# Optimization experiments

Measured on AMD Instinct MI355X. Metric: run time of the kernel, lower is better.

The kernel has to match this reference:

```python
import jax, jax.numpy as jnp
import numpy as np

N_NODES = 100000
N_EDGES = 2000000
H = 128


def setup_inputs() -> dict:
    key = jax.random.key(0)
    ks = jax.random.split(key, 5)
    z_src = jax.random.normal(ks[0], (N_NODES, H), dtype=jnp.float32)
    z_dst = jax.random.normal(ks[1], (N_NODES, H), dtype=jnp.float32)
    edge_label_index = jax.random.randint(ks[2], (2, N_EDGES), 0, N_NODES, dtype=jnp.int64)
    # Linear(2H, H) and Linear(H, 1) params (stored as [in, out] for x @ W)
    W1 = jax.random.normal(ks[3], (2 * H, H), dtype=jnp.float32) * (1.0 / np.sqrt(2 * H))
    b1 = jnp.zeros((H,), dtype=jnp.float32)
    W2 = jax.random.normal(ks[4], (H, 1), dtype=jnp.float32) * (1.0 / np.sqrt(H))
    b2 = jnp.zeros((1,), dtype=jnp.float32)
    return {"z_src": z_src, "z_dst": z_dst, "edge_label_index": edge_label_index,
            "W1": W1, "b1": b1, "W2": W2, "b2": b2}


def reference(z_src, z_dst, edge_label_index, W1, b1, W2, b2):
    row, col = edge_label_index[0], edge_label_index[1]
    # gather + concat -> [E, 2H]
    z = jnp.concatenate([z_src[row], z_dst[col]], axis=-1)
    h = jax.nn.relu(z @ W1 + b1)          # [E, H]
    out = h @ W2 + b2                     # [E, 1]
    return out.reshape(-1)
```

## Files before the change

### kernel.cpp

```cpp
#include <hip/hip_runtime.h>

#define HDIM 128
#define ZP   136
#define NBH  512

typedef __bf16 bf16_t;
typedef bf16_t bf16x8 __attribute__((ext_vector_type(8)));
typedef float  f32x4  __attribute__((ext_vector_type(4)));

__device__ __forceinline__ unsigned short f2bf_rne(float f) {
    unsigned int u = __float_as_uint(f);
    u += 0x7fffu + ((u >> 16) & 1u);
    return (unsigned short)(u >> 16);
}
__device__ __forceinline__ unsigned int pk_bf2(float a, float b) {
    return (unsigned int)f2bf_rne(a) | ((unsigned int)f2bf_rne(b) << 16);
}

__global__ __launch_bounds__(256) void convert_w1(
    const float* __restrict__ W1, unsigned short* __restrict__ Wt)
{
    const int o = blockIdx.x * 256 + threadIdx.x;
    const int g = o >> 14, rem = o & 16383, n = rem >> 7, k = rem & 127;
    Wt[o] = f2bf_rne(W1[g * 16384 + k * 128 + n]);
}

__global__ __launch_bounds__(256) void node_gemm_v3(
    const float* __restrict__ Zs, const float* __restrict__ Zd,
    const unsigned short* __restrict__ Wt, const float* __restrict__ b1,
    unsigned short* __restrict__ Abuf, unsigned short* __restrict__ Bbuf,
    int M)
{
    __shared__ unsigned short wlds[128 * ZP];

    const bool second = (blockIdx.x >= NBH);
    const float* __restrict__ Z          = second ? Zd : Zs;
    const unsigned short* __restrict__ W = Wt + (second ? 128 * 128 : 0);
    unsigned short* __restrict__ C       = second ? Bbuf : Abuf;
    const int bx = second ? (blockIdx.x - NBH) : blockIdx.x;
    const int t  = threadIdx.x;

    #pragma unroll
    for (int j = 0; j < 8; ++j) {
        const int u = t + 256 * j;
        const int n = u >> 4, c = u & 15;
        const uint4 v = *reinterpret_cast<const uint4*>(W + n * 128 + c * 8);
        *reinterpret_cast<uint4*>(wlds + n * ZP + c * 8) = v;
    }
    __syncthreads();

    const int lane = t & 63;
    const int wave = t >> 6;
    const int m    = lane & 15;
    const int quad = lane >> 4;

    const int ntiles = (M + 63) >> 6;
    for (int tile = bx; tile < ntiles; tile += NBH) {
        const int row0 = tile * 64;
        const int r    = row0 + wave * 16 + m;
        const int rc   = (r < M) ? r : (M - 1);
        const float* zrow = Z + (size_t)rc * HDIM;

        f32x4 acc[8] = {};
        #pragma unroll
        for (int ks = 0; ks < 4; ++ks) {
            const float4 v0 = *reinterpret_cast<const float4*>(zrow + ks * 32 + quad * 8);
            const float4 v1 = *reinterpret_cast<const float4*>(zrow + ks * 32 + quad * 8 + 4);
            union { unsigned int u[4]; bf16x8 h; } zf;
            zf.u[0] = pk_bf2(v0.x, v0.y);
            zf.u[1] = pk_bf2(v0.z, v0.w);
            zf.u[2] = pk_bf2(v1.x, v1.y);
            zf.u[3] = pk_bf2(v1.z, v1.w);
            #pragma unroll
            for (int ct = 0; ct < 8; ++ct) {
                const bf16x8 wf = *reinterpret_cast<const bf16x8*>(
                    wlds + (ct * 16 + m) * ZP + ks * 32 + quad * 8);
                acc[ct] = __builtin_amdgcn_mfma_f32_16x16x32_bf16(wf, zf.h, acc[ct], 0, 0, 0);
            }
        }

        if (r < M) {
            unsigned short* crow = C + (size_t)r * HDIM;
            #pragma unroll
            for (int ct = 0; ct < 8; ++ct) {
                const int col = ct * 16 + quad * 4;
                float4 bv = make_float4(0.f, 0.f, 0.f, 0.f);
                if (second) bv = *reinterpret_cast<const float4*>(b1 + col);
                uint2 o;
                o.x = pk_bf2(acc[ct][0] + bv.x, acc[ct][1] + bv.y);
                o.y = pk_bf2(acc[ct][2] + bv.z, acc[ct][3] + bv.w);
                *reinterpret_cast<uint2*>(crow + col) = o;
            }
        }
    }
}

__global__ __launch_bounds__(256) void edge_decode_bf16(
    const unsigned short* __restrict__ A, const unsigned short* __restrict__ Bm,
    const int* __restrict__ idx,
    const float* __restrict__ W2, const float* __restrict__ b2,
    float* __restrict__ out, int E)
{
    const int t   = threadIdx.x;
    const int sub = t & 15;
    const int grp = t >> 4;

    float w2r[8];
    #pragma unroll
    for (int i = 0; i < 8; ++i) w2r[i] = W2[sub * 8 + i];
    const float b2s = b2[0];

    const int stride = gridDim.x * 16;
    for (int e = blockIdx.x * 16 + grp; e < E; e += stride) {
        const int r = idx[e];
        const int c = idx[E + e];
        const uint4 av = *reinterpret_cast<const uint4*>(A  + (size_t)r * HDIM + sub * 8);
        const uint4 bv = *reinterpret_cast<const uint4*>(Bm + (size_t)c * HDIM + sub * 8);

        float s = 0.f;
        #pragma unroll
        for (int i = 0; i < 4; ++i) {
            const unsigned int ua = (&av.x)[i];
            const unsigned int ub = (&bv.x)[i];
            s += fmaxf(__uint_as_float(ua << 16)         + __uint_as_float(ub << 16),         0.f) * w2r[2 * i];
            s += fmaxf(__uint_as_float(ua & 0xffff0000u) + __uint_as_float(ub & 0xffff0000u), 0.f) * w2r[2 * i + 1];
        }
        s += __shfl_xor(s, 1);
        s += __shfl_xor(s, 2);
        s += __shfl_xor(s, 4);
        s += __shfl_xor(s, 8);
        if (sub == 0) out[e] = s + b2s;
    }
}

extern "C" void kernel_launch(void* const* d_in, const int* in_sizes, int n_in,
                              void* d_out, int out_size, void* d_ws, size_t ws_size,
                              hipStream_t stream)
{
    const float* z_src = (const float*)d_in[0];
    const float* z_dst = (const float*)d_in[1];
    const int*   eidx  = (const int*)d_in[2];
    const float* W1    = (const float*)d_in[3];
    const float* b1    = (const float*)d_in[4];
    const float* W2    = (const float*)d_in[5];
    const float* b2    = (const float*)d_in[6];
    float*       outp  = (float*)d_out;

    const int Nn = in_sizes[0] / HDIM;
    const int E  = in_sizes[2] / 2;

    unsigned short* Abuf = (unsigned short*)d_ws;
    unsigned short* Bbuf = Abuf + (size_t)Nn * HDIM;
    unsigned short* Wt   = Bbuf + (size_t)Nn * HDIM;

    convert_w1<<<128, 256, 0, stream>>>(W1, Wt);

    node_gemm_v3<<<2 * NBH, 256, 0, stream>>>(z_src, z_dst, Wt, b1, Abuf, Bbuf, Nn);

    edge_decode_bf16<<<8192, 256, 0, stream>>>(Abuf, Bbuf, eidx, W2, b2, outp, E);
}
```

Baseline: 292.2 us.

## Bucket-sort edges by source node before decode to improve gather locality

Adds a counting-sort pipeline (histogram, scan, atomic scatter) that groups edges into buckets of 128 source nodes, storing (row, col, edge id) records. The decode kernel then reads these sorted records so that source-row gathers from A hit cache better, and writes its output scattered by the original edge id. This adds four kernel launches, extra passes over the index array, a 32 MB sorted buffer, global atomics, and scattered output writes. The destination-side gathers stay random.

Result: slower. 766.7 us (+162.4%).

```diff
diff --git a/kernel.cpp b/kernel.cpp
--- a/kernel.cpp
+++ b/kernel.cpp
@@ -1,8 +1,9 @@
 #include <hip/hip_runtime.h>
 
-#define HDIM 128
-#define ZP   136
-#define NBH  512
+#define HDIM  128
+#define ZP    136
+#define NBH   512
+#define NBUCK 1024
 
 typedef __bf16 bf16_t;
 typedef bf16_t bf16x8 __attribute__((ext_vector_type(8)));
@@ -56,9 +57,8 @@
 
     const int ntiles = (M + 63) >> 6;
     for (int tile = bx; tile < ntiles; tile += NBH) {
-        const int row0 = tile * 64;
-        const int r    = row0 + wave * 16 + m;
-        const int rc   = (r < M) ? r : (M - 1);
+        const int r  = tile * 64 + wave * 16 + m;
+        const int rc = (r < M) ? r : (M - 1);
         const float* zrow = Z + (size_t)rc * HDIM;
 
         f32x4 acc[8] = {};
@@ -95,9 +95,58 @@
     }
 }
 
-__global__ __launch_bounds__(256) void edge_decode_bf16(
+__global__ __launch_bounds__(256) void zero_buf(int* __restrict__ p, int n)
+{
+    const int i = blockIdx.x * 256 + threadIdx.x;
+    if (i < n) p[i] = 0;
+}
+
+__global__ __launch_bounds__(256) void edge_hist(
+    const int* __restrict__ idx, int E, int* __restrict__ hist)
+{
+    __shared__ int h[NBUCK];
+    for (int i = threadIdx.x; i < NBUCK; i += 256) h[i] = 0;
+    __syncthreads();
+    const int stride = gridDim.x * 256;
+    for (int e = blockIdx.x * 256 + threadIdx.x; e < E; e += stride)
+        atomicAdd(&h[idx[e] >> 7], 1);
+    __syncthreads();
+    for (int i = threadIdx.x; i < NBUCK; i += 256)
+        if (h[i]) atomicAdd(&hist[i], h[i]);
+}
+
+__global__ __launch_bounds__(1024) void scan_hist(
+    const int* __restrict__ hist, int* __restrict__ cursor)
+{
+    __shared__ int a[NBUCK], b[NBUCK];
+    const int t = threadIdx.x;
+    a[t] = hist[t];
+    __syncthreads();
+    int* src = a; int* dst = b;
+    for (int off = 1; off < NBUCK; off <<= 1) {
+        dst[t] = (t >= off) ? (src[t - off] + src[t]) : src[t];
+        __syncthreads();
+        int* tmp = src; src = dst; dst = tmp;
+    }
+    cursor[t] = (t == 0) ? 0 : src[t - 1];
+}
+
+__global__ __launch_bounds__(256) void edge_scatter(
+    const int* __restrict__ idx, int E, int* __restrict__ cursor,
+    uint4* __restrict__ sorted)
+{
+    const int stride = gridDim.x * 256;
+    for (int e = blockIdx.x * 256 + threadIdx.x; e < E; e += stride) {
+        const int r = idx[e];
+        const int c = idx[E + e];
+        const int pos = atomicAdd(&cursor[r >> 7], 1);
+        sorted[pos] = make_uint4((unsigned)r, (unsigned)c, (unsigned)e, 0u);
+    }
+}
+
+__global__ __launch_bounds__(256) void edge_decode_sorted(
     const unsigned short* __restrict__ A, const unsigned short* __restrict__ Bm,
-    const int* __restrict__ idx,
+    const uint4* __restrict__ sorted,
     const float* __restrict__ W2, const float* __restrict__ b2,
     float* __restrict__ out, int E)
 {
@@ -111,11 +160,10 @@
     const float b2s = b2[0];
 
     const int stride = gridDim.x * 16;
-    for (int e = blockIdx.x * 16 + grp; e < E; e += stride) {
-        const int r = idx[e];
-        const int c = idx[E + e];
-        const uint4 av = *reinterpret_cast<const uint4*>(A  + (size_t)r * HDIM + sub * 8);
-        const uint4 bv = *reinterpret_cast<const uint4*>(Bm + (size_t)c * HDIM + sub * 8);
+    for (int g = blockIdx.x * 16 + grp; g < E; g += stride) {
+        const uint4 srt = sorted[g];
+        const uint4 av = *reinterpret_cast<const uint4*>(A  + (size_t)srt.x * HDIM + sub * 8);
+        const uint4 bv = *reinterpret_cast<const uint4*>(Bm + (size_t)srt.y * HDIM + sub * 8);
 
         float s = 0.f;
         #pragma unroll
@@ -129,7 +177,7 @@
         s += __shfl_xor(s, 2);
         s += __shfl_xor(s, 4);
         s += __shfl_xor(s, 8);
-        if (sub == 0) out[e] = s + b2s;
+        if (sub == 0) out[srt.z] = s + b2s;
     }
 }
 
@@ -152,10 +200,17 @@
     unsigned short* Abuf = (unsigned short*)d_ws;
     unsigned short* Bbuf = Abuf + (size_t)Nn * HDIM;
     unsigned short* Wt   = Bbuf + (size_t)Nn * HDIM;
+    int*            hist = (int*)(Wt + 2 * HDIM * HDIM);
+    int*          cursor = hist + NBUCK;
+    uint4*        sorted = (uint4*)(cursor + NBUCK);
 
     convert_w1<<<128, 256, 0, stream>>>(W1, Wt);
-
     node_gemm_v3<<<2 * NBH, 256, 0, stream>>>(z_src, z_dst, Wt, b1, Abuf, Bbuf, Nn);
 
-    edge_decode_bf16<<<8192, 256, 0, stream>>>(Abuf, Bbuf, eidx, W2, b2, outp, E);
-}
+    zero_buf<<<(NBUCK + 255) / 256, 256, 0, stream>>>(hist, NBUCK);
+    edge_hist<<<256, 256, 0, stream>>>(eidx, E, hist);
+    scan_hist<<<1, 1024, 0, stream>>>(hist, cursor);
+    edge_scatter<<<256, 256, 0, stream>>>(eidx, E, cursor, sorted);
+
+    edge_decode_sorted<<<8192, 256, 0, stream>>>(Abuf, Bbuf, sorted, W2, b2, outp, E);
+}
```
